# Optimization experiments

Hardware: AMD Instinct MI355X
Metric: run time of the kernel (lower is better)

The kernel has to match this reference:

```python
import jax, jax.numpy as jnp
import numpy as np

H = 768          # hidden_size
NH = 12          # num_attention_heads
DH = H // NH     # attention_head_size = 64
NE_TYPES = 16    # num_edge_types
B, S = 4, 512
N = B * S        # flattened node count
E = 131072       # number of edges


def setup_inputs() -> dict:
    key = jax.random.key(0)
    ks = jax.random.split(key, 12)
    inp = {
        "hidden_states": jax.random.normal(ks[0], (B, S, H), dtype=jnp.float32),
        "Wq": jax.random.normal(ks[1], (H, H), dtype=jnp.float32) * 0.02,
        "bq": jnp.zeros((H,), dtype=jnp.float32),
        "Wk": jax.random.normal(ks[2], (H, H), dtype=jnp.float32) * 0.02,
        "bk": jnp.zeros((H,), dtype=jnp.float32),
        "Wv": jax.random.normal(ks[3], (H, H), dtype=jnp.float32) * 0.02,
        "bv": jnp.zeros((H,), dtype=jnp.float32),
        "rel_key_emb": jax.random.normal(ks[4], (NE_TYPES, DH), dtype=jnp.float32) * 0.02,
        "rel_val_emb": jax.random.normal(ks[5], (NE_TYPES, DH), dtype=jnp.float32) * 0.02,
        "edges_src": jax.random.randint(ks[6], (E,), 0, N, dtype=jnp.int32),
        "edges_tgt": jax.random.randint(ks[7], (E,), 0, N, dtype=jnp.int32),
        "edges_type": jax.random.randint(ks[8], (E,), 0, NE_TYPES, dtype=jnp.int32),
        "edges_pos": jax.random.randint(ks[9], (E,), 0, NE_TYPES, dtype=jnp.int32),
    }
    return inp


def reference(hidden_states, Wq, bq, Wk, bk, Wv, bv, rel_key_emb, rel_val_emb,
              edges_src, edges_tgt, edges_type, edges_pos):
    b, s, h = hidden_states.shape
    n = b * s
    hs = hidden_states.reshape(n, h)
    # Q/K/V projections, split into heads: [N, NH, DH]
    q = (hs @ Wq.T + bq).reshape(n, NH, DH)
    k = (hs @ Wk.T + bk).reshape(n, NH, DH)
    v = (hs @ Wv.T + bv).reshape(n, NH, DH)
    # Edge gather + relative key embedding (broadcast over heads)
    src_key = k[edges_src] + rel_key_emb[edges_pos][:, None, :]      # [E, NH, DH]
    tgt_query = q[edges_tgt]                                          # [E, NH, DH]
    # Unnormalized exp attention scores per edge per head: [E, NH]
    scores = jnp.exp(jnp.sum(tgt_query * src_key, axis=-1) / jnp.sqrt(jnp.float32(DH)))
    # Segment softmax normalization via scatter-add over target nodes
    denom = jax.ops.segment_sum(scores, edges_tgt, num_segments=n)    # [N, NH]
    attn = scores / denom[edges_tgt]                                  # [E, NH]
    # Reweighted per-edge values (the meaningful computed quantity)
    src_val = v[edges_src] + rel_val_emb[edges_pos][:, None, :]       # [E, NH, DH]
    weighted = src_val * attn[:, :, None]                             # [E, NH, DH]
    # NOTE: the original torch forward returns hidden_states unchanged
    # (the attention chain is dead code). We return the computed edge-weighted
    # values as the correctness target for the gather->exp->scatter-softmax chain.
    return weighted
```

## Files before the change

### kernel.cpp

```cpp
#include <hip/hip_runtime.h>
#include <hip/hip_bf16.h>

#define H 768
#define NH 12
#define DH 64
#define NNODES 2048
#define NEDGES 131072

typedef __bf16 bf16x8 __attribute__((ext_vector_type(8)));
typedef float floatx4 __attribute__((ext_vector_type(4)));

#define GLOAD_LDS16(gptr, ldsptr)                                                        \
  __builtin_amdgcn_global_load_lds((const __attribute__((address_space(1))) void*)(gptr), \
                                   (__attribute__((address_space(3))) void*)(ldsptr),     \
                                   16, 0, 0)

__device__ __forceinline__ unsigned short f2bf(float x) {
  union { __hip_bfloat16 h; unsigned short u; } cv;
  cv.h = __float2bfloat16(x);
  return cv.u;
}

__device__ __forceinline__ float bfu2f(unsigned short u) {
  union { float f; unsigned int i; } c;
  c.i = ((unsigned int)u) << 16;
  return c.f;
}

__global__ __launch_bounds__(256)
void convert_kernel(const float* __restrict__ hs,
                    const float* __restrict__ Wq,
                    const float* __restrict__ Wk,
                    const float* __restrict__ Wv,
                    __hip_bfloat16* __restrict__ hsb,
                    __hip_bfloat16* __restrict__ wb,
                    int* __restrict__ hist) {
  int i = blockIdx.x * 256 + threadIdx.x;
  const int n_hs4 = NNODES * H / 4;
  const int n_w4  = H * H / 4;
  if (i < n_hs4) {
    float4 v = ((const float4*)hs)[i];
    ((ushort4*)hsb)[i] = make_ushort4(f2bf(v.x), f2bf(v.y), f2bf(v.z), f2bf(v.w));
    return;
  }
  int j = i - n_hs4;
  if (j < 3 * n_w4) {
    const float* src = (j < n_w4) ? Wq : (j < 2 * n_w4 ? Wk : Wv);
    float4 v = ((const float4*)src)[j % n_w4];
    ((ushort4*)wb)[j] = make_ushort4(f2bf(v.x), f2bf(v.y), f2bf(v.z), f2bf(v.w));
    return;
  }
  int z = j - 3 * n_w4;
  if (z < NNODES / 4) {
    ((int4*)hist)[z] = make_int4(0, 0, 0, 0);
  }
}

__global__ __launch_bounds__(256)
void qkv_gemm(const __hip_bfloat16* __restrict__ A,
              const __hip_bfloat16* __restrict__ Wb,
              const float* __restrict__ b0,
              const float* __restrict__ b1,
              const float* __restrict__ b2,
              float* __restrict__ out,
              __hip_bfloat16* __restrict__ kb) {
  __shared__ __hip_bfloat16 As[64][32];
  __shared__ __hip_bfloat16 Bs[64][32];

  const int t    = threadIdx.x;
  const int wave = t >> 6;
  const int lane = t & 63;
  const int bm   = blockIdx.x * 64;
  const int bn   = blockIdx.y * 64;
  const int mat  = blockIdx.z;

  const __hip_bfloat16* B = Wb + (size_t)mat * H * H;
  const float* bias = (mat == 0) ? b0 : ((mat == 1) ? b1 : b2);

  const int wm = (wave & 1) * 32;
  const int wn = (wave >> 1) * 32;
  const int lr = lane & 15;
  const int lq = lane >> 4;

  floatx4 acc[2][2] = {};

  const int ar = t >> 2;
  const int ac = (t & 3) * 8;
  __hip_bfloat16* AsF = &As[0][0];
  __hip_bfloat16* BsF = &Bs[0][0];

  for (int kt = 0; kt < H; kt += 32) {
    GLOAD_LDS16(A + (size_t)(bm + ar) * H + kt + ac, AsF + t * 8);
    GLOAD_LDS16(B + (size_t)(bn + ar) * H + kt + ac, BsF + t * 8);
    __syncthreads();

    bf16x8 af[2], bfr[2];
#pragma unroll
    for (int i = 0; i < 2; i++)
      af[i] = *(const bf16x8*)&As[wm + i * 16 + lr][lq * 8];
#pragma unroll
    for (int i = 0; i < 2; i++)
      bfr[i] = *(const bf16x8*)&Bs[wn + i * 16 + lr][lq * 8];
#pragma unroll
    for (int mi = 0; mi < 2; mi++)
#pragma unroll
      for (int ni = 0; ni < 2; ni++)
        acc[mi][ni] = __builtin_amdgcn_mfma_f32_16x16x32_bf16(
            af[mi], bfr[ni], acc[mi][ni], 0, 0, 0);
    __syncthreads();
  }

  if (mat == 1) {
#pragma unroll
    for (int ni = 0; ni < 2; ni++) {
      int col = bn + wn + ni * 16 + lr;
      float bv = bias[col];
#pragma unroll
      for (int mi = 0; mi < 2; mi++) {
#pragma unroll
        for (int r = 0; r < 4; r++) {
          int row = bm + wm + mi * 16 + lq * 4 + r;
          kb[(size_t)row * H + col] = __float2bfloat16(acc[mi][ni][r] + bv);
        }
      }
    }
  } else {
    float* C = out + (size_t)mat * NNODES * H;
#pragma unroll
    for (int ni = 0; ni < 2; ni++) {
      int col = bn + wn + ni * 16 + lr;
      float bv = bias[col];
#pragma unroll
      for (int mi = 0; mi < 2; mi++) {
#pragma unroll
        for (int r = 0; r < 4; r++) {
          int row = bm + wm + mi * 16 + lq * 4 + r;
          C[(size_t)row * H + col] = acc[mi][ni][r] + bv;
        }
      }
    }
  }
}

__global__ __launch_bounds__(256)
void hist_kernel(const int* __restrict__ etgt, int* __restrict__ hist) {
  int e = blockIdx.x * 256 + threadIdx.x;
  atomicAdd(&hist[etgt[e]], 1);
}

__global__ __launch_bounds__(256)
void scan_kernel(const int* __restrict__ hist, int* __restrict__ rowptr,
                 int* __restrict__ cursor) {
  __shared__ int part[256];
  int t = threadIdx.x;
  int loc[8];
  int s = 0;
#pragma unroll
  for (int k = 0; k < 8; k++) { loc[k] = s; s += hist[t * 8 + k]; }
  part[t] = s;
  __syncthreads();
  for (int off = 1; off < 256; off <<= 1) {
    int v = (t >= off) ? part[t - off] : 0;
    __syncthreads();
    if (t >= off) part[t] += v;
    __syncthreads();
  }
  int pre = part[t] - s;
#pragma unroll
  for (int k = 0; k < 8; k++) {
    rowptr[t * 8 + k] = pre + loc[k];
    cursor[t * 8 + k] = pre + loc[k];
  }
  if (t == 255) rowptr[NNODES] = part[255];
}

__global__ __launch_bounds__(256)
void scatter_kernel(const int* __restrict__ esrc, const int* __restrict__ etgt,
                    const int* __restrict__ epos,
                    int* __restrict__ cursor,
                    int* __restrict__ src_s, int* __restrict__ pos_s,
                    int* __restrict__ eorig) {
  int e = blockIdx.x * 256 + threadIdx.x;
  int tgt = etgt[e];
  int slot = atomicAdd(&cursor[tgt], 1);
  src_s[slot] = esrc[e];
  pos_s[slot] = epos[e];
  eorig[slot] = e;
}

__global__ __launch_bounds__(256)
void edge_fused_kernel(const float* __restrict__ Q,
                       const __hip_bfloat16* __restrict__ Kb,
                       const float* __restrict__ V,
                       const float* __restrict__ relk,
                       const float* __restrict__ relv,
                       const int* __restrict__ rowptr,
                       const int* __restrict__ src_s,
                       const int* __restrict__ pos_s,
                       const int* __restrict__ eorig,
                       float* __restrict__ scores_s,
                       float* __restrict__ out) {
  const int t    = blockIdx.x;
  const int tid  = threadIdx.x;
  const int wave = tid >> 6;
  const int lane = tid & 63;
  const int g    = lane >> 4;
  const int off  = (lane & 15) * 4;

  __shared__ float Qs[H];
  __shared__ float Rs[16 * DH];
  __shared__ float dpart[4][NH];
  __shared__ float dinv[NH];

  if (tid < 192)
    *(float4*)&Qs[tid * 4] = *(const float4*)(Q + (size_t)t * H + tid * 4);
  *(float4*)&Rs[tid * 4] = *(const float4*)(relk + tid * 4);
  __syncthreads();

  const int beg = rowptr[t], end = rowptr[t + 1];
  float dacc0 = 0.f, dacc1 = 0.f, dacc2 = 0.f;

  for (int i = beg + wave; i < end; i += 4) {
    const int src = src_s[i];
    const int pos = pos_s[i];
    const unsigned short* Kp = (const unsigned short*)(Kb + (size_t)src * H);
    const float4 r4 = *(const float4*)&Rs[pos * DH + off];
    float s[3];
#pragma unroll
    for (int c = 0; c < 3; c++) {
      ushort4 ku = *(const ushort4*)(Kp + c * 256 + lane * 4);
      float4 q4 = *(const float4*)&Qs[c * 256 + lane * 4];
      s[c] = q4.x * (bfu2f(ku.x) + r4.x) + q4.y * (bfu2f(ku.y) + r4.y) +
             q4.z * (bfu2f(ku.z) + r4.z) + q4.w * (bfu2f(ku.w) + r4.w);
    }
#pragma unroll
    for (int m = 1; m < 16; m <<= 1) {
      s[0] += __shfl_xor(s[0], m);
      s[1] += __shfl_xor(s[1], m);
      s[2] += __shfl_xor(s[2], m);
    }
    if ((lane & 15) == 0) {
      float sc0 = __expf(s[0] * 0.125f);
      float sc1 = __expf(s[1] * 0.125f);
      float sc2 = __expf(s[2] * 0.125f);
      scores_s[(size_t)i * NH + g]     = sc0;
      scores_s[(size_t)i * NH + 4 + g] = sc1;
      scores_s[(size_t)i * NH + 8 + g] = sc2;
      dacc0 += sc0; dacc1 += sc1; dacc2 += sc2;
    }
  }

  if ((lane & 15) == 0) {
    dpart[wave][g]     = dacc0;
    dpart[wave][4 + g] = dacc1;
    dpart[wave][8 + g] = dacc2;
  }
  __syncthreads();

  *(float4*)&Rs[tid * 4] = *(const float4*)(relv + tid * 4);
  if (tid < NH) {
    float den = dpart[0][tid] + dpart[1][tid] + dpart[2][tid] + dpart[3][tid];
    dinv[tid] = 1.0f / den;
  }
  __syncthreads();

  for (int i = beg + wave; i < end; i += 4) {
    const int src = src_s[i];
    const int pos = pos_s[i];
    const int e   = eorig[i];
    const float4 r4 = *(const float4*)&Rs[pos * DH + off];
#pragma unroll
    for (int c = 0; c < 3; c++) {
      int h = c * 4 + g;
      float a = scores_s[(size_t)i * NH + h] * dinv[h];
      float4 v4 = *(const float4*)(V + (size_t)src * H + c * 256 + lane * 4);
      floatx4 o;
      o.x = (v4.x + r4.x) * a;
      o.y = (v4.y + r4.y) * a;
      o.z = (v4.z + r4.z) * a;
      o.w = (v4.w + r4.w) * a;
      __builtin_nontemporal_store(
          o, (floatx4*)(out + (size_t)e * H + c * 256 + lane * 4));
    }
  }
}

extern "C" void kernel_launch(void* const* d_in, const int* in_sizes, int n_in,
                              void* d_out, int out_size, void* d_ws, size_t ws_size,
                              hipStream_t stream) {
  const float* hs   = (const float*)d_in[0];
  const float* Wq   = (const float*)d_in[1];
  const float* bq   = (const float*)d_in[2];
  const float* Wk   = (const float*)d_in[3];
  const float* bk   = (const float*)d_in[4];
  const float* Wv   = (const float*)d_in[5];
  const float* bv   = (const float*)d_in[6];
  const float* relk = (const float*)d_in[7];
  const float* relv = (const float*)d_in[8];
  const int* esrc   = (const int*)d_in[9];
  const int* etgt   = (const int*)d_in[10];
  const int* epos   = (const int*)d_in[12];
  float* out = (float*)d_out;

  char* ws = (char*)d_ws;
  __hip_bfloat16* hsb = (__hip_bfloat16*)ws;
  __hip_bfloat16* wb  = (__hip_bfloat16*)(ws + 3145728);
  float* qkv      = (float*)(ws + 6684672);
  float* scores_s = (float*)(ws + 25559040);
  int* hist       = (int*)(ws + 31948800);
  int* rowptr     = (int*)(ws + 31956992);
  int* cursor     = (int*)(ws + 31965200);
  __hip_bfloat16* kb = (__hip_bfloat16*)(ws + 31973392);
  int* src_s = (int*)ws;
  int* pos_s = (int*)(ws + 524288);
  int* eorig = (int*)(ws + 1048576);

  convert_kernel<<<3266, 256, 0, stream>>>(hs, Wq, Wk, Wv, hsb, wb, hist);

  dim3 grid_gemm(32, 12, 3);
  qkv_gemm<<<grid_gemm, 256, 0, stream>>>(hsb, wb, bq, bk, bv, qkv, kb);

  const float* Qp = qkv;
  const float* Vp = qkv + (size_t)2 * NNODES * H;

  hist_kernel<<<NEDGES / 256, 256, 0, stream>>>(etgt, hist);
  scan_kernel<<<1, 256, 0, stream>>>(hist, rowptr, cursor);
  scatter_kernel<<<NEDGES / 256, 256, 0, stream>>>(esrc, etgt, epos, cursor,
                                                   src_s, pos_s, eorig);

  edge_fused_kernel<<<NNODES, 256, 0, stream>>>(Qp, kb, Vp, relk, relv, rowptr,
                                                src_s, pos_s, eorig,
                                                scores_s, out);
}
```

Measured before the change: 526.3 us.

## Split edge kernel into per-target scores and per-source output passes

Builds a second CSR grouped by source node and splits the fused edge kernel in two. The first kernel computes scores per target and normalizes them in place. The second iterates edges per source so each block loads its V row into shared memory once, instead of gathering V rows per edge. This adds a second histogram, scan and atomic scatter, an extra kernel launch, and an indirect read of attention weights through the stored slot index.

New measurement: 553.7 us. 5.2% more time.

```diff
diff --git a/kernel.cpp b/kernel.cpp
--- a/kernel.cpp
+++ b/kernel.cpp
@@ -34,7 +34,7 @@
                     const float* __restrict__ Wv,
                     __hip_bfloat16* __restrict__ hsb,
                     __hip_bfloat16* __restrict__ wb,
-                    int* __restrict__ hist) {
+                    int* __restrict__ hists) {
   int i = blockIdx.x * 256 + threadIdx.x;
   const int n_hs4 = NNODES * H / 4;
   const int n_w4  = H * H / 4;
@@ -51,8 +51,8 @@
     return;
   }
   int z = j - 3 * n_w4;
-  if (z < NNODES / 4) {
-    ((int4*)hist)[z] = make_int4(0, 0, 0, 0);
+  if (z < 2 * NNODES / 4) {
+    ((int4*)hists)[z] = make_int4(0, 0, 0, 0);
   }
 }
 
@@ -143,63 +143,90 @@
 }
 
 __global__ __launch_bounds__(256)
-void hist_kernel(const int* __restrict__ etgt, int* __restrict__ hist) {
+void hist_kernel(const int* __restrict__ etgt, const int* __restrict__ esrc,
+                 int* __restrict__ hist1, int* __restrict__ hist2) {
   int e = blockIdx.x * 256 + threadIdx.x;
-  atomicAdd(&hist[etgt[e]], 1);
-}
-
-__global__ __launch_bounds__(256)
-void scan_kernel(const int* __restrict__ hist, int* __restrict__ rowptr,
-                 int* __restrict__ cursor) {
+  atomicAdd(&hist1[etgt[e]], 1);
+  atomicAdd(&hist2[esrc[e]], 1);
+}
+
+__global__ __launch_bounds__(256)
+void scan_kernel(const int* __restrict__ hist1, int* __restrict__ rowptr1,
+                 int* __restrict__ cursor1,
+                 const int* __restrict__ hist2, int* __restrict__ rowptr2,
+                 int* __restrict__ cursor2) {
   __shared__ int part[256];
   int t = threadIdx.x;
-  int loc[8];
-  int s = 0;
-#pragma unroll
-  for (int k = 0; k < 8; k++) { loc[k] = s; s += hist[t * 8 + k]; }
-  part[t] = s;
+
+  {
+    int loc[8]; int s = 0;
+#pragma unroll
+    for (int k = 0; k < 8; k++) { loc[k] = s; s += hist1[t * 8 + k]; }
+    part[t] = s;
+    __syncthreads();
+    for (int off = 1; off < 256; off <<= 1) {
+      int v = (t >= off) ? part[t - off] : 0;
+      __syncthreads();
+      if (t >= off) part[t] += v;
+      __syncthreads();
+    }
+    int pre = part[t] - s;
+#pragma unroll
+    for (int k = 0; k < 8; k++) {
+      rowptr1[t * 8 + k] = pre + loc[k];
+      cursor1[t * 8 + k] = pre + loc[k];
+    }
+    if (t == 255) rowptr1[NNODES] = part[255];
+  }
   __syncthreads();
-  for (int off = 1; off < 256; off <<= 1) {
-    int v = (t >= off) ? part[t - off] : 0;
+  {
+    int loc[8]; int s = 0;
+#pragma unroll
+    for (int k = 0; k < 8; k++) { loc[k] = s; s += hist2[t * 8 + k]; }
+    part[t] = s;
     __syncthreads();
-    if (t >= off) part[t] += v;
-    __syncthreads();
-  }
-  int pre = part[t] - s;
-#pragma unroll
-  for (int k = 0; k < 8; k++) {
-    rowptr[t * 8 + k] = pre + loc[k];
-    cursor[t * 8 + k] = pre + loc[k];
-  }
-  if (t == 255) rowptr[NNODES] = part[255];
+    for (int off = 1; off < 256; off <<= 1) {
+      int v = (t >= off) ? part[t - off] : 0;
+      __syncthreads();
+      if (t >= off) part[t] += v;
+      __syncthreads();
+    }
+    int pre = part[t] - s;
+#pragma unroll
+    for (int k = 0; k < 8; k++) {
+      rowptr2[t * 8 + k] = pre + loc[k];
+      cursor2[t * 8 + k] = pre + loc[k];
+    }
+    if (t == 255) rowptr2[NNODES] = part[255];
+  }
 }
 
 __global__ __launch_bounds__(256)
 void scatter_kernel(const int* __restrict__ esrc, const int* __restrict__ etgt,
                     const int* __restrict__ epos,
-                    int* __restrict__ cursor,
+                    int* __restrict__ cursor1, int* __restrict__ cursor2,
                     int* __restrict__ src_s, int* __restrict__ pos_s,
-                    int* __restrict__ eorig) {
+                    int* __restrict__ tslot2, int* __restrict__ pos2,
+                    int* __restrict__ eorig2) {
   int e = blockIdx.x * 256 + threadIdx.x;
-  int tgt = etgt[e];
-  int slot = atomicAdd(&cursor[tgt], 1);
-  src_s[slot] = esrc[e];
-  pos_s[slot] = epos[e];
-  eorig[slot] = e;
-}
-
-__global__ __launch_bounds__(256)
-void edge_fused_kernel(const float* __restrict__ Q,
-                       const __hip_bfloat16* __restrict__ Kb,
-                       const float* __restrict__ V,
-                       const float* __restrict__ relk,
-                       const float* __restrict__ relv,
-                       const int* __restrict__ rowptr,
-                       const int* __restrict__ src_s,
-                       const int* __restrict__ pos_s,
-                       const int* __restrict__ eorig,
-                       float* __restrict__ scores_s,
-                       float* __restrict__ out) {
+  int tgt = etgt[e], src = esrc[e], pos = epos[e];
+  int s1 = atomicAdd(&cursor1[tgt], 1);
+  src_s[s1] = src;
+  pos_s[s1] = pos;
+  int s2 = atomicAdd(&cursor2[src], 1);
+  tslot2[s2] = s1;
+  pos2[s2]   = pos;
+  eorig2[s2] = e;
+}
+
+__global__ __launch_bounds__(256)
+void edge_scores_kernel(const float* __restrict__ Q,
+                        const __hip_bfloat16* __restrict__ Kb,
+                        const float* __restrict__ relk,
+                        const int* __restrict__ rowptr1,
+                        const int* __restrict__ src_s,
+                        const int* __restrict__ pos_s,
+                        float* __restrict__ attn) {
   const int t    = blockIdx.x;
   const int tid  = threadIdx.x;
   const int wave = tid >> 6;
@@ -208,23 +235,23 @@
   const int off  = (lane & 15) * 4;
 
   __shared__ float Qs[H];
-  __shared__ float Rs[16 * DH];
+  __shared__ float Rk[16 * DH];
   __shared__ float dpart[4][NH];
   __shared__ float dinv[NH];
 
   if (tid < 192)
     *(float4*)&Qs[tid * 4] = *(const float4*)(Q + (size_t)t * H + tid * 4);
-  *(float4*)&Rs[tid * 4] = *(const float4*)(relk + tid * 4);
+  *(float4*)&Rk[tid * 4] = *(const float4*)(relk + tid * 4);
   __syncthreads();
 
-  const int beg = rowptr[t], end = rowptr[t + 1];
+  const int beg = rowptr1[t], end = rowptr1[t + 1];
   float dacc0 = 0.f, dacc1 = 0.f, dacc2 = 0.f;
 
   for (int i = beg + wave; i < end; i += 4) {
     const int src = src_s[i];
     const int pos = pos_s[i];
     const unsigned short* Kp = (const unsigned short*)(Kb + (size_t)src * H);
-    const float4 r4 = *(const float4*)&Rs[pos * DH + off];
+    const float4 r4 = *(const float4*)&Rk[pos * DH + off];
     float s[3];
 #pragma unroll
     for (int c = 0; c < 3; c++) {
@@ -243,9 +270,9 @@
       float sc0 = __expf(s[0] * 0.125f);
       float sc1 = __expf(s[1] * 0.125f);
       float sc2 = __expf(s[2] * 0.125f);
-      scores_s[(size_t)i * NH + g]     = sc0;
-      scores_s[(size_t)i * NH + 4 + g] = sc1;
-      scores_s[(size_t)i * NH + 8 + g] = sc2;
+      attn[(size_t)i * NH + g]     = sc0;
+      attn[(size_t)i * NH + 4 + g] = sc1;
+      attn[(size_t)i * NH + 8 + g] = sc2;
       dacc0 += sc0; dacc1 += sc1; dacc2 += sc2;
     }
   }
@@ -257,23 +284,57 @@
   }
   __syncthreads();
 
-  *(float4*)&Rs[tid * 4] = *(const float4*)(relv + tid * 4);
   if (tid < NH) {
     float den = dpart[0][tid] + dpart[1][tid] + dpart[2][tid] + dpart[3][tid];
     dinv[tid] = 1.0f / den;
   }
   __syncthreads();
 
-  for (int i = beg + wave; i < end; i += 4) {
-    const int src = src_s[i];
-    const int pos = pos_s[i];
-    const int e   = eorig[i];
-    const float4 r4 = *(const float4*)&Rs[pos * DH + off];
+  float4* aF4 = (float4*)attn;
+  const int b3 = beg * 3, e3 = end * 3;
+  for (int k4 = b3 + tid; k4 < e3; k4 += 256) {
+    int c = k4 % 3;
+    float4 v = aF4[k4];
+    float4 d = *(const float4*)&dinv[c * 4];
+    v.x *= d.x; v.y *= d.y; v.z *= d.z; v.w *= d.w;
+    aF4[k4] = v;
+  }
+}
+
+__global__ __launch_bounds__(256)
+void edge_out_kernel(const float* __restrict__ V,
+                     const float* __restrict__ relv,
+                     const int* __restrict__ rowptr2,
+                     const int* __restrict__ tslot2,
+                     const int* __restrict__ pos2,
+                     const int* __restrict__ eorig2,
+                     const float* __restrict__ attn,
+                     float* __restrict__ out) {
+  const int s    = blockIdx.x;
+  const int tid  = threadIdx.x;
+  const int wave = tid >> 6;
+  const int lane = tid & 63;
+  const int g    = lane >> 4;
+  const int off  = (lane & 15) * 4;
+
+  __shared__ float Vs[H];
+  __shared__ float Rv[16 * DH];
+
+  if (tid < 192)
+    *(float4*)&Vs[tid * 4] = *(const float4*)(V + (size_t)s * H + tid * 4);
+  *(float4*)&Rv[tid * 4] = *(const float4*)(relv + tid * 4);
+  __syncthreads();
+
+  const int beg = rowptr2[s], end = rowptr2[s + 1];
+  for (int j = beg + wave; j < end; j += 4) {
+    const int tslot = tslot2[j];
+    const int pos   = pos2[j];
+    const int e     = eorig2[j];
+    const float4 r4 = *(const float4*)&Rv[pos * DH + off];
 #pragma unroll
     for (int c = 0; c < 3; c++) {
-      int h = c * 4 + g;
-      float a = scores_s[(size_t)i * NH + h] * dinv[h];
-      float4 v4 = *(const float4*)(V + (size_t)src * H + c * 256 + lane * 4);
+      float a = attn[(size_t)tslot * NH + c * 4 + g];
+      float4 v4 = *(const float4*)&Vs[c * 256 + lane * 4];
       floatx4 o;
       o.x = (v4.x + r4.x) * a;
       o.y = (v4.y + r4.y) * a;
@@ -305,17 +366,22 @@
   char* ws = (char*)d_ws;
   __hip_bfloat16* hsb = (__hip_bfloat16*)ws;
   __hip_bfloat16* wb  = (__hip_bfloat16*)(ws + 3145728);
-  float* qkv      = (float*)(ws + 6684672);
-  float* scores_s = (float*)(ws + 25559040);
-  int* hist       = (int*)(ws + 31948800);
-  int* rowptr     = (int*)(ws + 31956992);
-  int* cursor     = (int*)(ws + 31965200);
-  __hip_bfloat16* kb = (__hip_bfloat16*)(ws + 31973392);
+  float* qkv   = (float*)(ws + 6684672);
+  float* attn  = (float*)(ws + 25559040);
+  int* hist1   = (int*)(ws + 31850496);
+  int* hist2   = (int*)(ws + 31858688);
+  int* rowptr1 = (int*)(ws + 31866880);
+  int* rowptr2 = (int*)(ws + 31875104);
+  int* cursor1 = (int*)(ws + 31883328);
+  int* cursor2 = (int*)(ws + 31891520);
+  __hip_bfloat16* kb = (__hip_bfloat16*)(ws + 31899712);
+  int* tslot2  = (int*)(ws + 35045440);
+  int* pos2    = (int*)(ws + 35569728);
+  int* eorig2  = (int*)(ws + 36094016);
   int* src_s = (int*)ws;
   int* pos_s = (int*)(ws + 524288);
-  int* eorig = (int*)(ws + 1048576);
-
-  convert_kernel<<<3266, 256, 0, stream>>>(hs, Wq, Wk, Wv, hsb, wb, hist);
+
+  convert_kernel<<<3268, 256, 0, stream>>>(hs, Wq, Wk, Wv, hsb, wb, hist1);
 
   dim3 grid_gemm(32, 12, 3);
   qkv_gemm<<<grid_gemm, 256, 0, stream>>>(hsb, wb, bq, bk, bv, qkv, kb);
@@ -323,12 +389,17 @@
   const float* Qp = qkv;
   const float* Vp = qkv + (size_t)2 * NNODES * H;
 
-  hist_kernel<<<NEDGES / 256, 256, 0, stream>>>(etgt, hist);
-  scan_kernel<<<1, 256, 0, stream>>>(hist, rowptr, cursor);
-  scatter_kernel<<<NEDGES / 256, 256, 0, stream>>>(esrc, etgt, epos, cursor,
-                                                   src_s, pos_s, eorig);
-
-  edge_fused_kernel<<<NNODES, 256, 0, stream>>>(Qp, kb, Vp, relk, relv, rowptr,
-                                                src_s, pos_s, eorig,
-                                                scores_s, out);
-}
+  hist_kernel<<<NEDGES / 256, 256, 0, stream>>>(etgt, esrc, hist1, hist2);
+  scan_kernel<<<1, 256, 0, stream>>>(hist1, rowptr1, cursor1,
+                                     hist2, rowptr2, cursor2);
+  scatter_kernel<<<NEDGES / 256, 256, 0, stream>>>(esrc, etgt, epos,
+                                                   cursor1, cursor2,
+                                                   src_s, pos_s,
+                                                   tslot2, pos2, eorig2);
+
+  edge_scores_kernel<<<NNODES, 256, 0, stream>>>(Qp, kb, relk, rowptr1,
+                                                 src_s, pos_s, attn);
+
+  edge_out_kernel<<<NNODES, 256, 0, stream>>>(Vp, relv, rowptr2, tslot2, pos2,
+                                              eorig2, attn, out);
+}
```
